# Kernel tuning notes

Hardware: AMD Instinct MI355X
Metric: run time of the kernel (lower is better)

The kernel has to match this reference:

```python
import jax, jax.numpy as jnp
import numpy as np

B, S, D, H = 2, 2048, 1024, 16
HD = D // H  # head_dim = 64


def setup_inputs() -> dict:
    key = jax.random.key(0)
    ks = jax.random.split(key, 9)
    s = 1.0 / np.sqrt(D)
    return {
        "x": jax.random.normal(ks[0], (B, S, D), dtype=jnp.float32),
        "Wq": jax.random.uniform(ks[1], (D, D), jnp.float32, -s, s),
        "bq": jnp.zeros((D,), jnp.float32),
        "Wk": jax.random.uniform(ks[2], (D, D), jnp.float32, -s, s),
        "bk": jnp.zeros((D,), jnp.float32),
        "Wv": jax.random.uniform(ks[3], (D, D), jnp.float32, -s, s),
        "bv": jnp.zeros((D,), jnp.float32),
        "Wo": jax.random.uniform(ks[4], (D, D), jnp.float32, -s, s),
        "bo": jnp.zeros((D,), jnp.float32),
    }


def reference(x, Wq, bq, Wk, bk, Wv, bv, Wo, bo):
    # x: [B,S,D] -> Q/K/V: [B,H,S,HD]
    def heads(t):
        return t.reshape(B, S, H, HD).transpose(0, 2, 1, 3)

    Q = heads(x @ Wq + bq)
    K = heads(x @ Wk + bk)
    V = heads(x @ Wv + bv)
    scale = jnp.sqrt(jnp.asarray(HD, dtype=x.dtype))
    energy = jnp.einsum("bhqd,bhkd->bhqk", Q, K) / scale  # [B,H,S,S]
    attn = jax.nn.softmax(energy, axis=-1)
    # dropout is identity in eval mode
    o = jnp.einsum("bhqk,bhkd->bhqd", attn, V)  # [B,H,S,HD]
    o = o.transpose(0, 2, 1, 3).reshape(B, S, D)
    return o @ Wo + bo
```

## Files before the change

### kernel.cpp

```cpp
#include <hip/hip_runtime.h>
#include <hip/hip_bf16.h>

#define B_  2
#define S_  2048
#define D_  1024
#define H_  16
#define HD_ 64

typedef __attribute__((ext_vector_type(8))) short bf16x8;
typedef __attribute__((ext_vector_type(4))) float f32x4;

typedef __attribute__((address_space(1))) const short gbl_short;
typedef __attribute__((address_space(3))) short lds_short;

__device__ __forceinline__ short f2bf(float f) {
  union { float f; unsigned u; } v; v.f = f;
  unsigned r = (v.u + 0x7FFFu + ((v.u >> 16) & 1u)) >> 16;
  return (short)r;
}

__device__ __forceinline__ short bf16s(float f) {
  __hip_bfloat16 h = __float2bfloat16(f);
  return *reinterpret_cast<short*>(&h);
}

__global__ __launch_bounds__(256) void cast_x_kernel(const float* __restrict__ x,
                                                     short* __restrict__ xb) {
  int i = blockIdx.x * 256 + threadIdx.x;
  float4 v = ((const float4*)x)[i];
  short4 o;
  o.x = f2bf(v.x); o.y = f2bf(v.y); o.z = f2bf(v.z); o.w = f2bf(v.w);
  ((short4*)xb)[i] = o;
}

__global__ __launch_bounds__(256) void transpose_cast_w(
    const float* __restrict__ w0, const float* __restrict__ w1,
    const float* __restrict__ w2, const float* __restrict__ w3,
    short* __restrict__ t0, short* __restrict__ t1,
    short* __restrict__ t2, short* __restrict__ t3) {
  const float* W = blockIdx.z == 0 ? w0 : blockIdx.z == 1 ? w1 : blockIdx.z == 2 ? w2 : w3;
  short* T       = blockIdx.z == 0 ? t0 : blockIdx.z == 1 ? t1 : blockIdx.z == 2 ? t2 : t3;
  __shared__ float tile[32][33];
  int tx = threadIdx.x, ty = threadIdx.y;
  int x0 = blockIdx.x * 32, y0 = blockIdx.y * 32;
#pragma unroll
  for (int i = 0; i < 4; ++i)
    tile[ty + i * 8][tx] = W[(y0 + ty + i * 8) * D_ + x0 + tx];
  __syncthreads();
#pragma unroll
  for (int i = 0; i < 4; ++i)
    T[(x0 + ty + i * 8) * D_ + y0 + tx] = f2bf(tile[tx][ty + i * 8]);
}

__global__ __launch_bounds__(256) void qkv_gemm(
    const short* __restrict__ xb,
    const short* __restrict__ Wqt, const short* __restrict__ Wkt, const short* __restrict__ Wvt,
    const float* __restrict__ bq, const float* __restrict__ bk, const float* __restrict__ bv,
    short* __restrict__ Qb, short* __restrict__ Kb, short* __restrict__ Vtb) {
  const int which = blockIdx.z;
  const short* Bt   = which == 0 ? Wqt : which == 1 ? Wkt : Wvt;
  const float* bias = which == 0 ? bq  : which == 1 ? bk  : bv;
  const float scl   = which == 0 ? 0.125f * 1.44269504089f : 1.0f;
  const int lane = threadIdx.x & 63, wave = threadIdx.x >> 6;
  const int l15 = lane & 15, quad = lane >> 4;
  const int wm = wave & 1, wn = wave >> 1;
  const int m0 = blockIdx.x * 128, n0 = blockIdx.y * 128;
  const int srow = lane >> 2;
  const int skp  = (lane & 3) * 8;

  __shared__ short lA[2][128 * 32];
  __shared__ short lB[2][128 * 32];

  f32x4 acc[4][4];
#pragma unroll
  for (int mi = 0; mi < 4; ++mi)
#pragma unroll
    for (int ni = 0; ni < 4; ++ni) { f32x4 z = {0.f, 0.f, 0.f, 0.f}; acc[mi][ni] = z; }

  auto stage = [&](int it, int buf) {
    int kk = it * 32;
#pragma unroll
    for (int j = 0; j < 2; ++j) {
      int c = wave * 2 + j;
      int row = c * 16 + srow;
      __builtin_amdgcn_global_load_lds(
          (gbl_short*)(xb + (m0 + row) * D_ + kk + skp),
          (lds_short*)(&lA[buf][0] + c * 512 + lane * 8), 16, 0, 0);
      __builtin_amdgcn_global_load_lds(
          (gbl_short*)(Bt + (n0 + row) * D_ + kk + skp),
          (lds_short*)(&lB[buf][0] + c * 512 + lane * 8), 16, 0, 0);
    }
  };

  stage(0, 0);
  __syncthreads();
  for (int it = 0; it < 32; ++it) {
    int cur = it & 1;
    if (it < 31) stage(it + 1, cur ^ 1);
    bf16x8 af[4], bf[4];
#pragma unroll
    for (int i = 0; i < 4; ++i) {
      af[i] = *(const bf16x8*)(&lA[cur][0] + (wm * 64 + i * 16 + l15) * 32 + quad * 8);
      bf[i] = *(const bf16x8*)(&lB[cur][0] + (wn * 64 + i * 16 + l15) * 32 + quad * 8);
    }
#pragma unroll
    for (int mi = 0; mi < 4; ++mi)
#pragma unroll
      for (int ni = 0; ni < 4; ++ni)
        acc[mi][ni] = __builtin_amdgcn_mfma_f32_16x16x32_bf16(af[mi], bf[ni], acc[mi][ni], 0, 0, 0);
    if (it < 31) __syncthreads();
  }

#pragma unroll
  for (int mi = 0; mi < 4; ++mi) {
    int m = m0 + wm * 64 + mi * 16 + quad * 4;
    int bb = m >> 11;
    int s0 = m & (S_ - 1);
#pragma unroll
    for (int ni = 0; ni < 4; ++ni) {
      int n = n0 + wn * 64 + ni * 16 + l15;
      int h = n >> 6, hd = n & 63;
      float bsv = bias[n];
      if (which < 2) {
        short* dst = which == 0 ? Qb : Kb;
#pragma unroll
        for (int r = 0; r < 4; ++r)
          dst[((bb * H_ + h) * S_ + (s0 + r)) * HD_ + hd] = f2bf((acc[mi][ni][r] + bsv) * scl);
      } else {
        short4 pk;
        pk.x = f2bf(acc[mi][ni][0] + bsv);
        pk.y = f2bf(acc[mi][ni][1] + bsv);
        pk.z = f2bf(acc[mi][ni][2] + bsv);
        pk.w = f2bf(acc[mi][ni][3] + bsv);
        *(short4*)(Vtb + ((bb * H_ + h) * HD_ + hd) * S_ + s0) = pk;
      }
    }
  }
}

__global__ __launch_bounds__(256) void out_gemm(
    const short* __restrict__ Ob, const short* __restrict__ Wot,
    const float* __restrict__ bo, float* __restrict__ out) {
  const int lane = threadIdx.x & 63, wave = threadIdx.x >> 6;
  const int l15 = lane & 15, quad = lane >> 4;
  const int m0 = blockIdx.x * 128, n0 = blockIdx.y * 64;
  const int srow = lane >> 2;
  const int skp  = (lane & 3) * 8;

  __shared__ short lA[2][128 * 32];
  __shared__ short lB[2][64 * 32];

  f32x4 acc[2][4];
#pragma unroll
  for (int mi = 0; mi < 2; ++mi)
#pragma unroll
    for (int ni = 0; ni < 4; ++ni) { f32x4 z = {0.f, 0.f, 0.f, 0.f}; acc[mi][ni] = z; }

  auto stage = [&](int it, int buf) {
    int kk = it * 32;
#pragma unroll
    for (int j = 0; j < 2; ++j) {
      int c = wave * 2 + j;
      __builtin_amdgcn_global_load_lds(
          (gbl_short*)(Ob + (m0 + c * 16 + srow) * D_ + kk + skp),
          (lds_short*)(&lA[buf][0] + c * 512 + lane * 8), 16, 0, 0);
    }
    __builtin_amdgcn_global_load_lds(
        (gbl_short*)(Wot + (n0 + wave * 16 + srow) * D_ + kk + skp),
        (lds_short*)(&lB[buf][0] + wave * 512 + lane * 8), 16, 0, 0);
  };

  stage(0, 0);
  __syncthreads();
  for (int it = 0; it < 32; ++it) {
    int cur = it & 1;
    if (it < 31) stage(it + 1, cur ^ 1);
    bf16x8 af[2], bf[4];
#pragma unroll
    for (int i = 0; i < 2; ++i)
      af[i] = *(const bf16x8*)(&lA[cur][0] + (wave * 32 + i * 16 + l15) * 32 + quad * 8);
#pragma unroll
    for (int i = 0; i < 4; ++i)
      bf[i] = *(const bf16x8*)(&lB[cur][0] + (i * 16 + l15) * 32 + quad * 8);
#pragma unroll
    for (int mi = 0; mi < 2; ++mi)
#pragma unroll
      for (int ni = 0; ni < 4; ++ni)
        acc[mi][ni] = __builtin_amdgcn_mfma_f32_16x16x32_bf16(af[mi], bf[ni], acc[mi][ni], 0, 0, 0);
    if (it < 31) __syncthreads();
  }

#pragma unroll
  for (int mi = 0; mi < 2; ++mi) {
    int m = m0 + wave * 32 + mi * 16 + quad * 4;
#pragma unroll
    for (int ni = 0; ni < 4; ++ni) {
      int n = n0 + ni * 16 + l15;
      float bsv = bo[n];
#pragma unroll
      for (int r = 0; r < 4; ++r)
        out[(m + r) * D_ + n] = acc[mi][ni][r] + bsv;
    }
  }
}

__global__ __launch_bounds__(512, 4) void attn_kernel(
    const short* __restrict__ Qb, const short* __restrict__ Kb,
    const short* __restrict__ Vtb, short* __restrict__ Ob) {
  const int qt = blockIdx.x, h = blockIdx.y, b = blockIdx.z;
  const int base = (b * H_ + h) * S_ * HD_;
  const int tid = threadIdx.x;
  const int lane = tid & 63, wave = tid >> 6;
  const int grp = wave >> 2;
  const int wq  = wave & 3;
  const int l15 = lane & 15, quad = lane >> 4;

  __shared__ __align__(16) char smem[51200];
  short* lK  = (short*)smem;
  short* lV  = (short*)(smem + 16384);
  short* lPw = (short*)(smem + 32768);

  const int q0 = qt * 128 + wq * 32;

  bf16x8 qf[2][2];
#pragma unroll
  for (int mi = 0; mi < 2; ++mi)
#pragma unroll
    for (int ks = 0; ks < 2; ++ks)
      qf[mi][ks] = *(const bf16x8*)(Qb + base + (q0 + mi * 16 + l15) * HD_ + ks * 32 + quad * 8);

  f32x4 oacc[2][4];
  f32x4 lacc[2];
#pragma unroll
  for (int mi = 0; mi < 2; ++mi) {
    f32x4 z = {0.f, 0.f, 0.f, 0.f};
    lacc[mi] = z;
#pragma unroll
    for (int nb = 0; nb < 4; ++nb) oacc[mi][nb] = z;
  }

  bf16x8 onesf;
#pragma unroll
  for (int i = 0; i < 8; ++i) onesf[i] = (short)0x3F80;

  const int tig  = tid & 255;
  const int slot = tig & 7;
  const int rbase = tig >> 3;
  const int sgrp = ((slot ^ (rbase & 7))) * 8;
  const short* kp = Kb + base + (grp * 1024 + rbase) * HD_ + sgrp;
  const short* vp = Vtb + base + rbase * S_ + grp * 1024 + sgrp;
  lds_short* ldk0 = (lds_short*)(lK + grp * 4096 + tig * 8);
  lds_short* ldv0 = (lds_short*)(lV + grp * 4096 + tig * 8);

  short* pw = lPw + wave * 1152;
  short* pbase = pw + quad * 4 * 72;
  const int swz = l15 & 7;

  for (int kt = 0; kt < 16; ++kt) {
#pragma unroll
    for (int j = 0; j < 2; ++j) {
      __builtin_amdgcn_global_load_lds((gbl_short*)(kp + j * 32 * HD_), ldk0 + j * 2048, 16, 0, 0);
      __builtin_amdgcn_global_load_lds((gbl_short*)(vp + j * 32 * S_),  ldv0 + j * 2048, 16, 0, 0);
    }
    kp += 64 * HD_;
    vp += 64;
    __syncthreads();

    f32x4 sacc[2][4];
#pragma unroll
    for (int mi = 0; mi < 2; ++mi)
#pragma unroll
      for (int nb = 0; nb < 4; ++nb) { f32x4 z = {0.f, 0.f, 0.f, 0.f}; sacc[mi][nb] = z; }
#pragma unroll
    for (int nb = 0; nb < 4; ++nb)
#pragma unroll
      for (int ks = 0; ks < 2; ++ks) {
        bf16x8 kf = *(const bf16x8*)(lK + grp * 4096 + (nb * 16 + l15) * 64 + (((ks * 4 + quad) ^ swz) * 8));
        sacc[0][nb] = __builtin_amdgcn_mfma_f32_16x16x32_bf16(qf[0][ks], kf, sacc[0][nb], 0, 0, 0);
        sacc[1][nb] = __builtin_amdgcn_mfma_f32_16x16x32_bf16(qf[1][ks], kf, sacc[1][nb], 0, 0, 0);
      }

    bf16x8 af[2][2];
#pragma unroll
    for (int mi = 0; mi < 2; ++mi) {
#pragma unroll
      for (int nb = 0; nb < 4; ++nb) {
        int cofs = ((nb ^ quad) * 16) + l15;
#pragma unroll
        for (int r = 0; r < 4; ++r)
          pbase[r * 72 + cofs] = bf16s(__builtin_amdgcn_exp2f(sacc[mi][nb][r]));
      }
#pragma unroll
      for (int ks = 0; ks < 2; ++ks)
        af[mi][ks] = *(const bf16x8*)(pw + l15 * 72 +
            (((ks * 2 + (quad >> 1)) ^ (l15 >> 2)) * 16) + (quad & 1) * 8);
    }

#pragma unroll
    for (int nbh = 0; nbh < 4; ++nbh)
#pragma unroll
      for (int ks = 0; ks < 2; ++ks) {
        bf16x8 vf = *(const bf16x8*)(lV + grp * 4096 + (nbh * 16 + l15) * 64 + (((ks * 4 + quad) ^ swz) * 8));
        oacc[0][nbh] = __builtin_amdgcn_mfma_f32_16x16x32_bf16(af[0][ks], vf, oacc[0][nbh], 0, 0, 0);
        oacc[1][nbh] = __builtin_amdgcn_mfma_f32_16x16x32_bf16(af[1][ks], vf, oacc[1][nbh], 0, 0, 0);
      }
#pragma unroll
    for (int mi = 0; mi < 2; ++mi) {
      lacc[mi] = __builtin_amdgcn_mfma_f32_16x16x32_bf16(af[mi][0], onesf, lacc[mi], 0, 0, 0);
      lacc[mi] = __builtin_amdgcn_mfma_f32_16x16x32_bf16(af[mi][1], onesf, lacc[mi], 0, 0, 0);
    }
    __syncthreads();
  }

  float* exch = (float*)smem;
  float* lex  = (float*)(smem + 32768);
  if (grp == 1) {
#pragma unroll
    for (int mi = 0; mi < 2; ++mi)
#pragma unroll
      for (int nbh = 0; nbh < 4; ++nbh)
#pragma unroll
        for (int r = 0; r < 4; ++r)
          exch[wq * 2048 + (mi * 16 + quad * 4 + r) * 64 + nbh * 16 + l15] = oacc[mi][nbh][r];
    if (l15 == 0) {
#pragma unroll
      for (int mi = 0; mi < 2; ++mi)
#pragma unroll
        for (int r = 0; r < 4; ++r)
          lex[wq * 32 + mi * 16 + quad * 4 + r] = lacc[mi][r];
    }
  }
  __syncthreads();
  if (grp == 0) {
#pragma unroll
    for (int mi = 0; mi < 2; ++mi)
#pragma unroll
      for (int r = 0; r < 4; ++r) {
        int row = mi * 16 + quad * 4 + r;
        float l2 = lex[wq * 32 + row];
        float inv = 1.0f / (lacc[mi][r] + l2);
        int sg = q0 + row;
#pragma unroll
        for (int nbh = 0; nbh < 4; ++nbh) {
          float o2 = exch[wq * 2048 + row * 64 + nbh * 16 + l15];
          Ob[(b * S_ + sg) * D_ + h * HD_ + nbh * 16 + l15] =
              bf16s((oacc[mi][nbh][r] + o2) * inv);
        }
      }
  }
}

extern "C" void kernel_launch(void* const* d_in, const int* in_sizes, int n_in,
                              void* d_out, int out_size, void* d_ws, size_t ws_size,
                              hipStream_t stream) {
  (void)in_sizes; (void)n_in; (void)out_size; (void)ws_size;
  const float* x  = (const float*)d_in[0];
  const float* Wq = (const float*)d_in[1];
  const float* bq = (const float*)d_in[2];
  const float* Wk = (const float*)d_in[3];
  const float* bk = (const float*)d_in[4];
  const float* Wv = (const float*)d_in[5];
  const float* bv = (const float*)d_in[6];
  const float* Wo = (const float*)d_in[7];
  const float* bo = (const float*)d_in[8];
  float* out = (float*)d_out;

  char* ws = (char*)d_ws;
  short* xb  = (short*)(ws);
  short* Wqt = (short*)(ws + 8388608);
  short* Wkt = Wqt + 1048576;
  short* Wvt = Wkt + 1048576;
  short* Wot = Wvt + 1048576;
  short* Qb  = Wot + 1048576;
  short* Kb  = Qb + 4194304;
  short* Vtb = Kb + 4194304;
  short* Ob  = Vtb + 4194304;

  cast_x_kernel<<<4096, 256, 0, stream>>>(x, xb);
  transpose_cast_w<<<dim3(32, 32, 4), dim3(32, 8), 0, stream>>>(
      Wq, Wk, Wv, Wo, Wqt, Wkt, Wvt, Wot);
  qkv_gemm<<<dim3(32, 8, 3), 256, 0, stream>>>(
      xb, Wqt, Wkt, Wvt, bq, bk, bv, Qb, Kb, Vtb);
  attn_kernel<<<dim3(16, 16, 2), 512, 0, stream>>>(Qb, Kb, Vtb, Ob);
  out_gemm<<<dim3(32, 16), 256, 0, stream>>>(Ob, Wot, bo, out);
}
```

Baseline: 199.2 us.

## Halve attention block size and double-buffer K/V tiles with 32-key steps

The attention kernel now uses 256-thread blocks covering 64 queries each, so the grid doubles. K/V tiles shrink to 32 keys per step per group and are double-buffered, with the next tile prefetched via global_load_lds while the current one is computed. This aims to overlap load latency with MFMA work and to raise occupancy through smaller blocks. In exchange, K/V is loaded twice as often across blocks, and the shrunken exchange region at the end must still fit the reduced shared-memory layout.

```diff
diff --git a/kernel.cpp b/kernel.cpp
--- a/kernel.cpp
+++ b/kernel.cpp
@@ -204,23 +204,23 @@
   }
 }
 
-__global__ __launch_bounds__(512, 4) void attn_kernel(
+__global__ __launch_bounds__(256, 4) void attn_kernel(
     const short* __restrict__ Qb, const short* __restrict__ Kb,
     const short* __restrict__ Vtb, short* __restrict__ Ob) {
   const int qt = blockIdx.x, h = blockIdx.y, b = blockIdx.z;
   const int base = (b * H_ + h) * S_ * HD_;
   const int tid = threadIdx.x;
   const int lane = tid & 63, wave = tid >> 6;
-  const int grp = wave >> 2;
-  const int wq  = wave & 3;
+  const int grp = wave >> 1;
+  const int wq  = wave & 1;
   const int l15 = lane & 15, quad = lane >> 4;
 
-  __shared__ __align__(16) char smem[51200];
+  __shared__ __align__(16) char smem[36864];
   short* lK  = (short*)smem;
   short* lV  = (short*)(smem + 16384);
   short* lPw = (short*)(smem + 32768);
 
-  const int q0 = qt * 128 + wq * 32;
+  const int q0 = qt * 64 + wq * 32;
 
   bf16x8 qf[2][2];
 #pragma unroll
@@ -243,77 +243,77 @@
 #pragma unroll
   for (int i = 0; i < 8; ++i) onesf[i] = (short)0x3F80;
 
-  const int tig  = tid & 255;
-  const int slot = tig & 7;
-  const int rbase = tig >> 3;
-  const int sgrp = ((slot ^ (rbase & 7))) * 8;
-  const short* kp = Kb + base + (grp * 1024 + rbase) * HD_ + sgrp;
-  const short* vp = Vtb + base + rbase * S_ + grp * 1024 + sgrp;
-  lds_short* ldk0 = (lds_short*)(lK + grp * 4096 + tig * 8);
-  lds_short* ldv0 = (lds_short*)(lV + grp * 4096 + tig * 8);
-
-  short* pw = lPw + wave * 1152;
-  short* pbase = pw + quad * 4 * 72;
-  const int swz = l15 & 7;
-
-  for (int kt = 0; kt < 16; ++kt) {
+  const int tig = tid & 127;
+  const int slotK = tig & 7,  rowK = tig >> 3;
+  const int slotV = tig & 3,  rowV = tig >> 2;
+  const short* kp = Kb + base + (grp * 1024 + rowK) * HD_ + ((slotK ^ (rowK & 7)) * 8);
+  const short* vp = Vtb + base + rowV * S_ + grp * 1024 + ((slotV ^ (rowV & 3)) * 8);
+  lds_short* ldk = (lds_short*)(lK + grp * 2048 + tig * 8);
+  lds_short* ldv = (lds_short*)(lV + grp * 2048 + tig * 8);
+
+  auto stage = [&](int kt, int buf) {
 #pragma unroll
     for (int j = 0; j < 2; ++j) {
-      __builtin_amdgcn_global_load_lds((gbl_short*)(kp + j * 32 * HD_), ldk0 + j * 2048, 16, 0, 0);
-      __builtin_amdgcn_global_load_lds((gbl_short*)(vp + j * 32 * S_),  ldv0 + j * 2048, 16, 0, 0);
-    }
-    kp += 64 * HD_;
-    vp += 64;
-    __syncthreads();
-
-    f32x4 sacc[2][4];
+      __builtin_amdgcn_global_load_lds((gbl_short*)(kp + kt * 32 * HD_ + j * 16 * HD_),
+                                       ldk + buf * 4096 + j * 1024, 16, 0, 0);
+      __builtin_amdgcn_global_load_lds((gbl_short*)(vp + kt * 32 + j * 32 * S_),
+                                       ldv + buf * 4096 + j * 1024, 16, 0, 0);
+    }
+  };
+
+  short* pwv = lPw + wave * 512;
+  const int swzK = l15 & 7;
+  const int swzV = l15 & 3;
+
+  stage(0, 0);
+  __syncthreads();
+
+  for (int kt = 0; kt < 32; ++kt) {
+    const int buf = kt & 1;
+    if (kt < 31) stage(kt + 1, buf ^ 1);
+
+    const short* lKc = lK + buf * 4096 + grp * 2048;
+    const short* lVc = lV + buf * 4096 + grp * 2048;
+
+    f32x4 sacc[2][2];
 #pragma unroll
     for (int mi = 0; mi < 2; ++mi)
 #pragma unroll
-      for (int nb = 0; nb < 4; ++nb) { f32x4 z = {0.f, 0.f, 0.f, 0.f}; sacc[mi][nb] = z; }
-#pragma unroll
-    for (int nb = 0; nb < 4; ++nb)
+      for (int nb = 0; nb < 2; ++nb) { f32x4 z = {0.f, 0.f, 0.f, 0.f}; sacc[mi][nb] = z; }
+#pragma unroll
+    for (int nb = 0; nb < 2; ++nb)
 #pragma unroll
       for (int ks = 0; ks < 2; ++ks) {
-        bf16x8 kf = *(const bf16x8*)(lK + grp * 4096 + (nb * 16 + l15) * 64 + (((ks * 4 + quad) ^ swz) * 8));
+        bf16x8 kf = *(const bf16x8*)(lKc + (nb * 16 + l15) * 64 + (((ks * 4 + quad) ^ swzK) * 8));
         sacc[0][nb] = __builtin_amdgcn_mfma_f32_16x16x32_bf16(qf[0][ks], kf, sacc[0][nb], 0, 0, 0);
         sacc[1][nb] = __builtin_amdgcn_mfma_f32_16x16x32_bf16(qf[1][ks], kf, sacc[1][nb], 0, 0, 0);
       }
 
-    bf16x8 af[2][2];
+    bf16x8 af[2];
 #pragma unroll
     for (int mi = 0; mi < 2; ++mi) {
 #pragma unroll
-      for (int nb = 0; nb < 4; ++nb) {
-        int cofs = ((nb ^ quad) * 16) + l15;
+      for (int nb = 0; nb < 2; ++nb)
 #pragma unroll
         for (int r = 0; r < 4; ++r)
-          pbase[r * 72 + cofs] = bf16s(__builtin_amdgcn_exp2f(sacc[mi][nb][r]));
-      }
-#pragma unroll
-      for (int ks = 0; ks < 2; ++ks)
-        af[mi][ks] = *(const bf16x8*)(pw + l15 * 72 +
-            (((ks * 2 + (quad >> 1)) ^ (l15 >> 2)) * 16) + (quad & 1) * 8);
-    }
-
-#pragma unroll
-    for (int nbh = 0; nbh < 4; ++nbh)
-#pragma unroll
-      for (int ks = 0; ks < 2; ++ks) {
-        bf16x8 vf = *(const bf16x8*)(lV + grp * 4096 + (nbh * 16 + l15) * 64 + (((ks * 4 + quad) ^ swz) * 8));
-        oacc[0][nbh] = __builtin_amdgcn_mfma_f32_16x16x32_bf16(af[0][ks], vf, oacc[0][nbh], 0, 0, 0);
-        oacc[1][nbh] = __builtin_amdgcn_mfma_f32_16x16x32_bf16(af[1][ks], vf, oacc[1][nbh], 0, 0, 0);
-      }
-#pragma unroll
-    for (int mi = 0; mi < 2; ++mi) {
-      lacc[mi] = __builtin_amdgcn_mfma_f32_16x16x32_bf16(af[mi][0], onesf, lacc[mi], 0, 0, 0);
-      lacc[mi] = __builtin_amdgcn_mfma_f32_16x16x32_bf16(af[mi][1], onesf, lacc[mi], 0, 0, 0);
-    }
+          pwv[(quad * 4 + r) * 32 + nb * 16 + l15] =
+              bf16s(__builtin_amdgcn_exp2f(sacc[mi][nb][r]));
+      af[mi] = *(const bf16x8*)(pwv + l15 * 32 + quad * 8);
+    }
+
+#pragma unroll
+    for (int nbh = 0; nbh < 4; ++nbh) {
+      bf16x8 vf = *(const bf16x8*)(lVc + (nbh * 16 + l15) * 32 + ((quad ^ swzV) * 8));
+      oacc[0][nbh] = __builtin_amdgcn_mfma_f32_16x16x32_bf16(af[0], vf, oacc[0][nbh], 0, 0, 0);
+      oacc[1][nbh] = __builtin_amdgcn_mfma_f32_16x16x32_bf16(af[1], vf, oacc[1][nbh], 0, 0, 0);
+    }
+    lacc[0] = __builtin_amdgcn_mfma_f32_16x16x32_bf16(af[0], onesf, lacc[0], 0, 0, 0);
+    lacc[1] = __builtin_amdgcn_mfma_f32_16x16x32_bf16(af[1], onesf, lacc[1], 0, 0, 0);
     __syncthreads();
   }
 
   float* exch = (float*)smem;
-  float* lex  = (float*)(smem + 32768);
+  float* lex  = (float*)(smem + 16384);
   if (grp == 1) {
 #pragma unroll
     for (int mi = 0; mi < 2; ++mi)
@@ -381,6 +381,6 @@
       Wq, Wk, Wv, Wo, Wqt, Wkt, Wvt, Wot);
   qkv_gemm<<<dim3(32, 8, 3), 256, 0, stream>>>(
       xb, Wqt, Wkt, Wvt, bq, bk, bv, Qb, Kb, Vtb);
-  attn_kernel<<<dim3(16, 16, 2), 512, 0, stream>>>(Qb, Kb, Vtb, Ob);
+  attn_kernel<<<dim3(32, 16, 2), 256, 0, stream>>>(Qb, Kb, Vtb, Ob);
   out_gemm<<<dim3(32, 16), 256, 0, stream>>>(Ob, Wot, bo, out);
 }
```

Result: slower. 207.5 us (+4.1%).
